# Kernel optimization log

Measured on AMD Instinct MI355X. Metric: run time of the kernel, lower is better.

The kernel has to match this reference:

```python
import jax, jax.numpy as jnp
import numpy as np

BIT = 4  # layer_bits
QMAX = 2 ** (BIT - 1) - 1  # 7


def setup_inputs() -> dict:
    key = jax.random.key(0)
    k_in, k_qw, k_fw, k_a, k_b, k_n, k_out = jax.random.split(key, 7)
    in_features, out_features, outlier_num = 8192, 8192, 256
    q_in = in_features - outlier_num  # 7936
    tokens = 64

    inp = jax.random.normal(k_in, (tokens, in_features), dtype=jnp.float32)
    q_w = jax.random.normal(k_qw, (out_features, q_in), dtype=jnp.float32)
    fp_w = jax.random.normal(k_fw, (out_features, outlier_num), dtype=jnp.float32)
    # alpha_scale: positive per-row clip scale (init ones in torch; use ~U(0.5,1.5))
    alpha = jax.random.uniform(k_a, (out_features, 1), dtype=jnp.float32) + 0.5
    bias = jax.random.normal(k_b, (out_features,), dtype=jnp.float32)
    noise = jax.random.normal(k_n, (out_features, q_in), dtype=jnp.float32)

    # build col_perm / inv_col_perm from a deterministic set of outlier column ids
    rng = np.random.RandomState(0)
    outlier_ids = rng.choice(in_features, size=outlier_num, replace=False)
    mask = np.ones(in_features, dtype=bool)
    mask[outlier_ids] = False
    col_ids = np.arange(in_features, dtype=np.int32)
    col_perm = np.concatenate([col_ids[mask], col_ids[~mask]])
    inv_col_perm = np.zeros_like(col_perm)
    inv_col_perm[col_perm] = np.arange(in_features, dtype=np.int32)

    return {
        "input": inp,
        "sasut_q_weight": q_w,
        "sasut_fp_weight": fp_w,
        "alpha_scale": alpha,
        "bias": bias,
        "noise": noise,
        "inv_col_perm": jnp.asarray(inv_col_perm),
    }


def reference(input, sasut_q_weight, sasut_fp_weight, alpha_scale, bias, noise, inv_col_perm):
    # BitNoiseQuant._compute_quant_noise, training path with trainable alpha:
    # delta = alpha / qmax ; normal noise -> randn/2
    w = sasut_q_weight
    delta = alpha_scale / QMAX                       # [out, 1]
    w_rand = (noise * 0.5) * delta                   # [out, q_in]
    w_noised = jnp.where(
        w >= alpha_scale,
        alpha_scale,
        jnp.where(w <= -alpha_scale, -alpha_scale, w + w_rand),
    )
    # hstack quantized + fp outlier blocks, then undo the column permutation
    out_w = jnp.concatenate([w_noised, sasut_fp_weight], axis=1)  # [out, in]
    out_w = out_w[:, inv_col_perm]
    # F.linear: input @ out_w.T + bias
    return input @ out_w.T + bias
```

## Files before the change

kernel.cpp:

```cpp
#include <hip/hip_runtime.h>

#define TOK    64
#define NOUT   8192
#define KTOT   8192
#define KQ     7936
#define KFP    256
#define NWAVE  8
#define WCH    (KTOT / NWAVE)
#define NS     (WCH / 32)

typedef float f32x4 __attribute__((ext_vector_type(4)));
typedef short s16x8 __attribute__((ext_vector_type(8)));

__device__ __forceinline__ unsigned short f2bf(float f) {
    unsigned int u = __float_as_uint(f);
    u += 0x7fffu + ((u >> 16) & 1u);
    return (unsigned short)(u >> 16);
}

__global__ void prep(const float* __restrict__ inp, const int* __restrict__ invp,
                     unsigned short* __restrict__ xp) {
    int idx = blockIdx.x * blockDim.x + threadIdx.x;
    int j = idx & (KTOT - 1);
    xp[(idx >> 13) * KTOT + invp[j]] = f2bf(inp[idx]);
}

__global__ __launch_bounds__(512, 4) void sasut_gemm(
    const unsigned short* __restrict__ xp,
    const float* __restrict__ qw,
    const float* __restrict__ fpw,
    const float* __restrict__ alpha,
    const float* __restrict__ noise,
    const float* __restrict__ bias,
    float* __restrict__ out)
{
    __shared__ float red[NWAVE][4][16][17];
    const int tid  = threadIdx.x;
    const int w    = tid >> 6;
    const int lane = tid & 63;
    const int nloc = lane & 15;
    const int quad = lane >> 4;
    const int nbase = blockIdx.x * 16;
    const int kw   = w * WCH;

    const int row = nbase + nloc;
    const float a_s  = alpha[row];
    const float c_s  = a_s * (1.0f / 14.0f);
    const float na_s = -a_s;

    const float* qp  = qw    + (size_t)row * KQ  + kw + quad * 8;
    const float* np  = noise + (size_t)row * KQ  + kw + quad * 8;
    const float* fpq = fpw   + (size_t)row * KFP + quad * 8;

    const unsigned short* x0 = xp + (size_t)nloc * KTOT + kw + quad * 8;
    const unsigned short* x1 = x0 + (size_t)16 * KTOT;
    const unsigned short* x2 = x0 + (size_t)32 * KTOT;
    const unsigned short* x3 = x0 + (size_t)48 * KTOT;

    f32x4 acc0 = {0.f, 0.f, 0.f, 0.f};
    f32x4 acc1 = acc0, acc2 = acc0, acc3 = acc0;

    #pragma unroll 2
    for (int s = 0; s < NS; ++s) {
        const int k_ = kw + s * 32;
        s16x8 a0f = *(const s16x8*)(x0 + s * 32);
        s16x8 a1f = *(const s16x8*)(x1 + s * 32);
        s16x8 a2f = *(const s16x8*)(x2 + s * 32);
        s16x8 a3f = *(const s16x8*)(x3 + s * 32);
        s16x8 bf;
        if (k_ < KQ) {
            f32x4 qa = *(const f32x4*)(qp + s * 32);
            f32x4 qc = *(const f32x4*)(qp + s * 32 + 4);
            f32x4 na = *(const f32x4*)(np + s * 32);
            f32x4 nc = *(const f32x4*)(np + s * 32 + 4);
            #pragma unroll
            for (int j = 0; j < 8; ++j) {
                float wv = (j < 4) ? qa[j] : qc[j - 4];
                float nz = (j < 4) ? na[j] : nc[j - 4];
                float t = fmaf(nz, c_s, wv);
                t = (wv >= a_s)  ? a_s  : t;
                t = (wv <= na_s) ? na_s : t;
                bf[j] = (short)f2bf(t);
            }
        } else {
            const float* f_ = fpq + (k_ - KQ);
            f32x4 qa = *(const f32x4*)(f_);
            f32x4 qc = *(const f32x4*)(f_ + 4);
            #pragma unroll
            for (int j = 0; j < 8; ++j) {
                float wv = (j < 4) ? qa[j] : qc[j - 4];
                bf[j] = (short)f2bf(wv);
            }
        }
        acc0 = __builtin_amdgcn_mfma_f32_16x16x32_bf16(a0f, bf, acc0, 0, 0, 0);
        acc1 = __builtin_amdgcn_mfma_f32_16x16x32_bf16(a1f, bf, acc1, 0, 0, 0);
        acc2 = __builtin_amdgcn_mfma_f32_16x16x32_bf16(a2f, bf, acc2, 0, 0, 0);
        acc3 = __builtin_amdgcn_mfma_f32_16x16x32_bf16(a3f, bf, acc3, 0, 0, 0);
    }

    #pragma unroll
    for (int r = 0; r < 4; ++r) {
        red[w][0][quad * 4 + r][nloc] = acc0[r];
        red[w][1][quad * 4 + r][nloc] = acc1[r];
        red[w][2][quad * 4 + r][nloc] = acc2[r];
        red[w][3][quad * 4 + r][nloc] = acc3[r];
    }
    __syncthreads();
    #pragma unroll
    for (int rep = 0; rep < 2; ++rep) {
        int e   = tid + rep * 512;
        int m   = e >> 8;
        int tl  = (e >> 4) & 15;
        int col = e & 15;
        float v = bias[nbase + col];
        #pragma unroll
        for (int ww = 0; ww < NWAVE; ++ww) v += red[ww][m][tl][col];
        out[(size_t)(m * 16 + tl) * NOUT + nbase + col] = v;
    }
}

extern "C" void kernel_launch(void* const* d_in, const int* in_sizes, int n_in,
                              void* d_out, int out_size, void* d_ws, size_t ws_size,
                              hipStream_t stream) {
    const float* inp   = (const float*)d_in[0];
    const float* qw    = (const float*)d_in[1];
    const float* fpw   = (const float*)d_in[2];
    const float* alpha = (const float*)d_in[3];
    const float* bias  = (const float*)d_in[4];
    const float* noise = (const float*)d_in[5];
    const int*   invp  = (const int*)d_in[6];
    float* out = (float*)d_out;
    unsigned short* xp = (unsigned short*)d_ws;

    prep<<<(TOK * KTOT) / 256, 256, 0, stream>>>(inp, invp, xp);
    sasut_gemm<<<512, 512, 0, stream>>>(xp, qw, fpw, alpha, noise, bias, out);
}
```

Baseline: 549.4 us.

## Stream weight/noise rows through double-buffered LDS via global_load_lds with swizzled layout

Reworks the GEMM so each block walks K in 256-wide stages: every wave issues row-contiguous direct-to-LDS loads (global_load_lds) of the weight and noise tiles into a double buffer with an XOR swizzle, and reads its fragments back from LDS. Activations are pre-packed by the prep kernel into a K-blocked layout so each stage's A fragments are contiguous, and they are prefetched one stage ahead in registers. The aim is long contiguous DRAM streams and overlap of the 512 MB fp32 weight/noise read with the dequant and MFMA work, replacing strided per-lane global loads. The cost is manual vmcnt bookkeeping and barriers every stage, plus 64 KB of LDS per block, which may limit occupancy.

Measured after the change: 515.9 us. -6.1%, faster.

```diff
diff --git a/kernel.cpp b/kernel.cpp
--- a/kernel.cpp
+++ b/kernel.cpp
@@ -1,13 +1,12 @@
 #include <hip/hip_runtime.h>
 
-#define TOK    64
-#define NOUT   8192
-#define KTOT   8192
-#define KQ     7936
-#define KFP    256
-#define NWAVE  8
-#define WCH    (KTOT / NWAVE)
-#define NS     (WCH / 32)
+#define TOK   64
+#define NOUT  8192
+#define KTOT  8192
+#define KQ    7936
+#define KFP   256
+#define SK    256
+#define NS    32
 
 typedef float f32x4 __attribute__((ext_vector_type(4)));
 typedef short s16x8 __attribute__((ext_vector_type(8)));
@@ -18,15 +17,24 @@
     return (unsigned short)(u >> 16);
 }
 
+__device__ __forceinline__ void gl16(const void* g, void* l) {
+    __builtin_amdgcn_global_load_lds(
+        (const __attribute__((address_space(1))) void*)g,
+        (__attribute__((address_space(3))) void*)l, 16, 0, 0);
+}
+
+#define WAITV(n) asm volatile("s_waitcnt vmcnt(" #n ")" ::: "memory")
+
 __global__ void prep(const float* __restrict__ inp, const int* __restrict__ invp,
-                     unsigned short* __restrict__ xp) {
+                     unsigned short* __restrict__ xq) {
     int idx = blockIdx.x * blockDim.x + threadIdx.x;
-    int j = idx & (KTOT - 1);
-    xp[(idx >> 13) * KTOT + invp[j]] = f2bf(inp[idx]);
+    int t = idx >> 13, c = idx & (KTOT - 1);
+    int p = invp[c];
+    xq[(size_t)((p >> 3) * TOK + t) * 8 + (p & 7)] = f2bf(inp[idx]);
 }
 
 __global__ __launch_bounds__(512, 4) void sasut_gemm(
-    const unsigned short* __restrict__ xp,
+    const unsigned short* __restrict__ xq,
     const float* __restrict__ qw,
     const float* __restrict__ fpw,
     const float* __restrict__ alpha,
@@ -34,45 +42,81 @@
     const float* __restrict__ bias,
     float* __restrict__ out)
 {
-    __shared__ float red[NWAVE][4][16][17];
+    __shared__ __attribute__((aligned(16))) char smem[2 * 32768];
     const int tid  = threadIdx.x;
     const int w    = tid >> 6;
     const int lane = tid & 63;
     const int nloc = lane & 15;
     const int quad = lane >> 4;
     const int nbase = blockIdx.x * 16;
-    const int kw   = w * WCH;
 
     const int row = nbase + nloc;
     const float a_s  = alpha[row];
     const float c_s  = a_s * (1.0f / 14.0f);
     const float na_s = -a_s;
 
-    const float* qp  = qw    + (size_t)row * KQ  + kw + quad * 8;
-    const float* np  = noise + (size_t)row * KQ  + kw + quad * 8;
-    const float* fpq = fpw   + (size_t)row * KFP + quad * 8;
+    const int rA = 2 * w, rB = 2 * w + 1;
+    const size_t qoffA = (size_t)(nbase + rA) * KQ  + ((lane ^ (rA & 7)) << 2);
+    const size_t qoffB = (size_t)(nbase + rB) * KQ  + ((lane ^ (rB & 7)) << 2);
+    const size_t foffA = (size_t)(nbase + rA) * KFP + ((lane ^ (rA & 7)) << 2);
+    const size_t foffB = (size_t)(nbase + rB) * KFP + ((lane ^ (rB & 7)) << 2);
 
-    const unsigned short* x0 = xp + (size_t)nloc * KTOT + kw + quad * 8;
-    const unsigned short* x1 = x0 + (size_t)16 * KTOT;
-    const unsigned short* x2 = x0 + (size_t)32 * KTOT;
-    const unsigned short* x3 = x0 + (size_t)48 * KTOT;
+    auto stage = [&](int s2) {
+        char* b = smem + (s2 & 1) * 32768;
+        if (s2 < NS - 1) {
+            const float* q = qw    + (size_t)s2 * SK;
+            const float* n = noise + (size_t)s2 * SK;
+            gl16(q + qoffA, b + rA * 1024);
+            gl16(q + qoffB, b + rB * 1024);
+            gl16(n + qoffA, b + 16384 + rA * 1024);
+            gl16(n + qoffB, b + 16384 + rB * 1024);
+        } else {
+            gl16(fpw + foffA, b + rA * 1024);
+            gl16(fpw + foffB, b + rB * 1024);
+        }
+    };
+
+    const int sw  = nloc & 7;
+    const int c0  = w * 8 + quad * 2;
+    const int cc0 = ((c0     ^ sw) << 2);
+    const int cc1 = (((c0+1) ^ sw) << 2);
+
+    const unsigned short* xA = xq + (size_t)(w * 4 + quad) * 512 + nloc * 8;
+
+    stage(0);
+    s16x8 a0 = *(const s16x8*)(xA);
+    s16x8 a1 = *(const s16x8*)(xA + 128);
+    s16x8 a2 = *(const s16x8*)(xA + 256);
+    s16x8 a3 = *(const s16x8*)(xA + 384);
+    stage(1);
 
     f32x4 acc0 = {0.f, 0.f, 0.f, 0.f};
     f32x4 acc1 = acc0, acc2 = acc0, acc3 = acc0;
 
-    #pragma unroll 2
     for (int s = 0; s < NS; ++s) {
-        const int k_ = kw + s * 32;
-        s16x8 a0f = *(const s16x8*)(x0 + s * 32);
-        s16x8 a1f = *(const s16x8*)(x1 + s * 32);
-        s16x8 a2f = *(const s16x8*)(x2 + s * 32);
-        s16x8 a3f = *(const s16x8*)(x3 + s * 32);
-        s16x8 bf;
-        if (k_ < KQ) {
-            f32x4 qa = *(const f32x4*)(qp + s * 32);
-            f32x4 qc = *(const f32x4*)(qp + s * 32 + 4);
-            f32x4 na = *(const f32x4*)(np + s * 32);
-            f32x4 nc = *(const f32x4*)(np + s * 32 + 4);
+        if (s == 0)          WAITV(4);
+        else if (s < NS - 2) WAITV(8);
+        else if (s == NS-2)  WAITV(6);
+        else                 WAITV(4);
+        __builtin_amdgcn_s_barrier();
+
+        s16x8 b0 = a0, b1 = a1, b2 = a2, b3 = a3;
+        if (s + 1 < NS) {
+            const unsigned short* p = xA + (size_t)(s + 1) * 16384;
+            b0 = *(const s16x8*)(p);
+            b1 = *(const s16x8*)(p + 128);
+            b2 = *(const s16x8*)(p + 256);
+            b3 = *(const s16x8*)(p + 384);
+        }
+
+        const float* qb = (const float*)(smem + (s & 1) * 32768) + nloc * 256;
+        f32x4 qa = *(const f32x4*)(qb + cc0);
+        f32x4 qc = *(const f32x4*)(qb + cc1);
+        s16x8 bfv;
+        if (s < NS - 1) {
+            const float* nb = qb + 4096;
+            f32x4 na = *(const f32x4*)(nb + cc0);
+            f32x4 nc = *(const f32x4*)(nb + cc1);
             #pragma unroll
             for (int j = 0; j < 8; ++j) {
                 float wv = (j < 4) ? qa[j] : qc[j - 4];
@@ -80,30 +124,33 @@
                 float t = fmaf(nz, c_s, wv);
                 t = (wv >= a_s)  ? a_s  : t;
                 t = (wv <= na_s) ? na_s : t;
-                bf[j] = (short)f2bf(t);
+                bfv[j] = (short)f2bf(t);
             }
         } else {
-            const float* f_ = fpq + (k_ - KQ);
-            f32x4 qa = *(const f32x4*)(f_);
-            f32x4 qc = *(const f32x4*)(f_ + 4);
             #pragma unroll
             for (int j = 0; j < 8; ++j) {
                 float wv = (j < 4) ? qa[j] : qc[j - 4];
-                bf[j] = (short)f2bf(wv);
+                bfv[j] = (short)f2bf(wv);
             }
         }
-        acc0 = __builtin_amdgcn_mfma_f32_16x16x32_bf16(a0f, bf, acc0, 0, 0, 0);
-        acc1 = __builtin_amdgcn_mfma_f32_16x16x32_bf16(a1f, bf, acc1, 0, 0, 0);
-        acc2 = __builtin_amdgcn_mfma_f32_16x16x32_bf16(a2f, bf, acc2, 0, 0, 0);
-        acc3 = __builtin_amdgcn_mfma_f32_16x16x32_bf16(a3f, bf, acc3, 0, 0, 0);
+        acc0 = __builtin_amdgcn_mfma_f32_16x16x32_bf16(a0, bfv, acc0, 0, 0, 0);
+        acc1 = __builtin_amdgcn_mfma_f32_16x16x32_bf16(a1, bfv, acc1, 0, 0, 0);
+        acc2 = __builtin_amdgcn_mfma_f32_16x16x32_bf16(a2, bfv, acc2, 0, 0, 0);
+        acc3 = __builtin_amdgcn_mfma_f32_16x16x32_bf16(a3, bfv, acc3, 0, 0, 0);
+
+        __builtin_amdgcn_s_barrier();
+        if (s + 2 < NS) stage(s + 2);
+        a0 = b0; a1 = b1; a2 = b2; a3 = b3;
     }
 
+    __syncthreads();
+    float* red = (float*)smem;
     #pragma unroll
     for (int r = 0; r < 4; ++r) {
-        red[w][0][quad * 4 + r][nloc] = acc0[r];
-        red[w][1][quad * 4 + r][nloc] = acc1[r];
-        red[w][2][quad * 4 + r][nloc] = acc2[r];
-        red[w][3][quad * 4 + r][nloc] = acc3[r];
+        red[((w * 4 + 0) * 16 + quad * 4 + r) * 17 + nloc] = acc0[r];
+        red[((w * 4 + 1) * 16 + quad * 4 + r) * 17 + nloc] = acc1[r];
+        red[((w * 4 + 2) * 16 + quad * 4 + r) * 17 + nloc] = acc2[r];
+        red[((w * 4 + 3) * 16 + quad * 4 + r) * 17 + nloc] = acc3[r];
     }
     __syncthreads();
     #pragma unroll
@@ -114,7 +161,8 @@
         int col = e & 15;
         float v = bias[nbase + col];
         #pragma unroll
-        for (int ww = 0; ww < NWAVE; ++ww) v += red[ww][m][tl][col];
+        for (int ww = 0; ww < 8; ++ww)
+            v += red[((ww * 4 + m) * 16 + tl) * 17 + col];
         out[(size_t)(m * 16 + tl) * NOUT + nbase + col] = v;
     }
 }
@@ -130,8 +178,8 @@
     const float* noise = (const float*)d_in[5];
     const int*   invp  = (const int*)d_in[6];
     float* out = (float*)d_out;
-    unsigned short* xp = (unsigned short*)d_ws;
+    unsigned short* xq = (unsigned short*)d_ws;
 
-    prep<<<(TOK * KTOT) / 256, 256, 0, stream>>>(inp, invp, xp);
-    sasut_gemm<<<512, 512, 0, stream>>>(xp, qw, fpw, alpha, noise, bias, out);
+    prep<<<(TOK * KTOT) / 256, 256, 0, stream>>>(inp, invp, xq);
+    sasut_gemm<<<NOUT / 16, 512, 0, stream>>>(xq, qw, fpw, alpha, noise, bias, out);
 }
```
